# Kernel optimization log

Measured on AMD Instinct MI355X. Metric: run time of the kernel, lower is better.

Reference implementation:

```python
import jax, jax.numpy as jnp
import numpy as np
from jax import lax

B, T, IN, H = 16384, 10, 160, 256


def _lstm_layer(x, W_ih, W_hh, b_ih, b_hh):
    # x: [B, T, in]; PyTorch gate order: i, f, g, o. W_ih: [4H, in], W_hh: [4H, H]
    xg = jnp.einsum('bti,gi->btg', x, W_ih) + b_ih  # [B, T, 4H] precomputed input contributions
    h0 = jnp.zeros((x.shape[0], H), x.dtype)
    c0 = jnp.zeros((x.shape[0], H), x.dtype)

    def step(carry, xg_t):
        h, c = carry
        g = xg_t + h @ W_hh.T + b_hh  # [B, 4H]
        i, f, gg, o = jnp.split(g, 4, axis=-1)
        i = jax.nn.sigmoid(i)
        f = jax.nn.sigmoid(f)
        gg = jnp.tanh(gg)
        o = jax.nn.sigmoid(o)
        c = f * c + i * gg
        h = o * jnp.tanh(c)
        return (h, c), h

    _, hs = lax.scan(step, (h0, c0), xg.transpose(1, 0, 2))  # hs: [T, B, H]
    return hs.transpose(1, 0, 2)  # [B, T, H]


def setup_inputs() -> dict:
    key = jax.random.key(0)
    ks = jax.random.split(key, 11)
    s = 1.0 / np.sqrt(H)  # PyTorch default init scale
    inp = {
        'x': jax.random.normal(ks[0], (B, T, IN), jnp.float32),
        'W_ih0': jax.random.normal(ks[1], (4 * H, IN), jnp.float32) * s,
        'W_hh0': jax.random.normal(ks[2], (4 * H, H), jnp.float32) * s,
        'b_ih0': jax.random.normal(ks[3], (4 * H,), jnp.float32) * s,
        'b_hh0': jax.random.normal(ks[4], (4 * H,), jnp.float32) * s,
        'W_ih1': jax.random.normal(ks[5], (4 * H, H), jnp.float32) * s,
        'W_hh1': jax.random.normal(ks[6], (4 * H, H), jnp.float32) * s,
        'b_ih1': jax.random.normal(ks[7], (4 * H,), jnp.float32) * s,
        'b_hh1': jax.random.normal(ks[8], (4 * H,), jnp.float32) * s,
        'W_fc': jax.random.normal(ks[9], (1, T * H), jnp.float32) * 0.02,
        'b_fc': jax.random.normal(ks[10], (1,), jnp.float32) * 0.02,
    }
    return inp


def reference(x, W_ih0, W_hh0, b_ih0, b_hh0, W_ih1, W_hh1, b_ih1, b_hh1, W_fc, b_fc):
    x = x.reshape(-1, T, IN)
    h1 = _lstm_layer(x, W_ih0, W_hh0, b_ih0, b_hh0)   # [B, T, H]
    h2 = _lstm_layer(h1, W_ih1, W_hh1, b_ih1, b_hh1)  # [B, T, H]
    flat = h2.reshape(-1, T * H)                      # [B, 2560]
    logits = flat @ W_fc.T + b_fc                     # [B, 1]
    return jax.nn.sigmoid(logits)
```

## Files before the change

kernel.cpp:

```cpp
#include <hip/hip_runtime.h>

#define NTHREADS 512

typedef __attribute__((ext_vector_type(8))) short s16x8;
typedef __attribute__((ext_vector_type(4))) float f32x4;
typedef __attribute__((ext_vector_type(4))) unsigned int u32x4;

__device__ __forceinline__ unsigned short f2bf(float f) {
  unsigned u = __float_as_uint(f);
  u += 0x7fffu + ((u >> 16) & 1u);
  return (unsigned short)(u >> 16);
}
__device__ __forceinline__ float bf2f(unsigned short s) {
  return __uint_as_float(((unsigned)s) << 16);
}
__device__ __forceinline__ float sigm(float x) {
  return __builtin_amdgcn_rcpf(1.0f + __expf(-x));
}
__device__ __forceinline__ float tanh_fast(float x) {
  return 1.0f - 2.0f * __builtin_amdgcn_rcpf(1.0f + __expf(2.0f * x));
}
__device__ __forceinline__ f32x4 mfma_bf16(u32x4 a, u32x4 b, f32x4 c) {
  union { u32x4 u; s16x8 s; } ua, ub;
  ua.u = a; ub.u = b;
  return __builtin_amdgcn_mfma_f32_16x16x32_bf16(ua.s, ub.s, c, 0, 0, 0);
}

__global__ void pack_weights(const float* __restrict__ Wih0, const float* __restrict__ Whh0,
                             const float* __restrict__ bih0, const float* __restrict__ bhh0,
                             const float* __restrict__ Wih1, const float* __restrict__ Whh1,
                             const float* __restrict__ bih1, const float* __restrict__ bhh1,
                             unsigned short* __restrict__ W0p, unsigned short* __restrict__ W1p,
                             float* __restrict__ b0, float* __restrict__ b1) {
  int e = blockIdx.x * 256 + threadIdx.x;
  const int N0 = 16 * 52 * 4 * 128;
  const int N1 = 16 * 64 * 4 * 128;
  if (e < N0) {
    int kk = e & 7, t1 = e >> 3;
    int n = t1 & 15, t2 = t1 >> 4;
    int g = t2 & 3, t3 = t2 >> 2;
    int kb = t3 % 52, nb = t3 / 52;
    int gn = g * 256 + nb * 16 + n, k = kb * 8 + kk;
    float v = (k < 160) ? Wih0[gn * 160 + k] : Whh0[gn * 256 + (k - 160)];
    W0p[e] = f2bf(v);
  } else if (e < N0 + N1) {
    int e2 = e - N0;
    int kk = e2 & 7, t1 = e2 >> 3;
    int n = t1 & 15, t2 = t1 >> 4;
    int g = t2 & 3, t3 = t2 >> 2;
    int kb = t3 & 63, nb = t3 >> 6;
    int gn = g * 256 + nb * 16 + n, k = kb * 8 + kk;
    float v = (k < 256) ? Wih1[gn * 256 + k] : Whh1[gn * 256 + (k - 256)];
    W1p[e2] = f2bf(v);
  } else if (e < N0 + N1 + 1024) {
    int n = e - (N0 + N1);
    b0[n] = bih0[n] + bhh0[n];
  } else if (e < N0 + N1 + 2048) {
    int n = e - (N0 + N1 + 1024);
    b1[n] = bih1[n] + bhh1[n];
  }
}

__device__ __forceinline__ void ld4(u32x4 d[4], const u32x4* p) {
  d[0] = p[0]; d[1] = p[16]; d[2] = p[32]; d[3] = p[48];
}
__device__ __forceinline__ void mfma16(const u32x4 a[4], const u32x4 b[4],
                                       f32x4 acc[4][4]) {
#pragma unroll
  for (int g = 0; g < 4; g++)
#pragma unroll
    for (int rt = 0; rt < 4; rt++)
      acc[g][rt] = mfma_bf16(a[rt], b[g], acc[g][rt]);
}
template <int N>
__device__ __forceinline__ void kloop(const u32x4*& ap, const u32x4*& wp,
                                      f32x4 acc[4][4]) {
  u32x4 a0[4], b0[4], a1[4], b1[4];
  ld4(a0, ap); ld4(b0, wp); ap += 256; wp += 256;
#pragma unroll 1
  for (int i = 0; i < (N - 1) / 2; i++) {
    ld4(a1, ap); ld4(b1, wp); ap += 256; wp += 256;
    mfma16(a0, b0, acc);
    ld4(a0, ap); ld4(b0, wp); ap += 256; wp += 256;
    mfma16(a1, b1, acc);
  }
  if constexpr ((N & 1) == 0) {
    ld4(a1, ap); ld4(b1, wp); ap += 256; wp += 256;
    mfma16(a0, b0, acc);
    mfma16(a1, b1, acc);
  } else {
    mfma16(a0, b0, acc);
  }
}

__global__ __attribute__((amdgpu_flat_work_group_size(NTHREADS, NTHREADS),
                          amdgpu_waves_per_eu(2, 2)))
void lstm_fused(const float* __restrict__ x,
                const unsigned short* __restrict__ W0p,
                const unsigned short* __restrict__ W1p,
                const float* __restrict__ b0,
                const float* __restrict__ b1,
                const float* __restrict__ Wfc,
                const float* __restrict__ bfc,
                float* __restrict__ out) {
  __shared__ unsigned int lds_x[20 * 64 * 4];
  __shared__ unsigned int lds_h1[16384];
  __shared__ unsigned int lds_h2[16384];
  __shared__ float lds_red[512];
  __shared__ float lds_b0[1024];
  __shared__ float lds_b1[1024];

  const int tid = threadIdx.x;
  const int wave = tid >> 6;
  const int lane = tid & 63;
  const int l15 = lane & 15;
  const int quad = lane >> 4;
  const long rowg0 = (long)blockIdx.x * 64;

  for (int i = tid; i < 16384; i += NTHREADS) { lds_h1[i] = 0u; lds_h2[i] = 0u; }
  for (int i = tid; i < 1024; i += NTHREADS) { lds_b0[i] = b0[i]; lds_b1[i] = b1[i]; }

  float c0A[4][4], c0B[4][4], c2A[4][4], c2B[4][4];
#pragma unroll
  for (int rt = 0; rt < 4; rt++)
#pragma unroll
    for (int r = 0; r < 4; r++) {
      c0A[rt][r] = 0.f; c0B[rt][r] = 0.f;
      c2A[rt][r] = 0.f; c2B[rt][r] = 0.f;
    }
  float fc_acc = 0.0f;

  const u32x4* lxs = (const u32x4*)lds_x;
  const u32x4* lh1 = (const u32x4*)lds_h1;
  const u32x4* lh2 = (const u32x4*)lds_h2;
  unsigned short* lh1s = (unsigned short*)lds_h1;
  unsigned short* lh2s = (unsigned short*)lds_h2;
  const u32x4* w0q = (const u32x4*)W0p;
  const u32x4* w1q = (const u32x4*)W1p;

  for (int t = 0; t < 10; t++) {
    const int rd = t & 1;
    const int wr = rd ^ 1;

#pragma unroll
    for (int s = 0; s < 5; s++) {
      int p = tid + s * NTHREADS;
      int row = p / 40;
      int kq = p - row * 40;
      const f32x4 v = __builtin_nontemporal_load(
          (const f32x4*)(x + (rowg0 + row) * 1600 + t * 160 + kq * 4));
      unsigned lo = (unsigned)f2bf(v[0]) | ((unsigned)f2bf(v[1]) << 16);
      unsigned hi = (unsigned)f2bf(v[2]) | ((unsigned)f2bf(v[3]) << 16);
      int base = (kq >> 1) * 256 + row * 4 + (kq & 1) * 2;
      lds_x[base] = lo;
      lds_x[base + 1] = hi;
    }
    __syncthreads();

#pragma unroll 1
    for (int jt = 0; jt < 2; jt++) {
      const int nbb = wave * 2 + jt;
      f32x4 acc[4][4];
#pragma unroll
      for (int g = 0; g < 4; g++)
#pragma unroll
        for (int rt = 0; rt < 4; rt++) acc[g][rt] = (f32x4){0.f, 0.f, 0.f, 0.f};

      const u32x4* wp = w0q + (nbb * 52 + quad) * 64 + l15;
      const u32x4* ap = lxs + quad * 64 + l15;
      kloop<5>(ap, wp, acc);
      ap = lh1 + rd * 2048 + quad * 64 + l15;
      kloop<8>(ap, wp, acc);

      float b_i = lds_b0[0 * 256 + wave * 32 + jt * 16 + l15];
      float b_f = lds_b0[1 * 256 + wave * 32 + jt * 16 + l15];
      float b_g = lds_b0[2 * 256 + wave * 32 + jt * 16 + l15];
      float b_o = lds_b0[3 * 256 + wave * 32 + jt * 16 + l15];
#pragma unroll
      for (int rt = 0; rt < 4; rt++)
#pragma unroll
        for (int r = 0; r < 4; r++) {
          float iv = sigm(acc[0][rt][r] + b_i);
          float fv = sigm(acc[1][rt][r] + b_f);
          float gv = tanh_fast(acc[2][rt][r] + b_g);
          float ov = sigm(acc[3][rt][r] + b_o);
          float cn = fv * c0A[rt][r] + iv * gv;
          c0A[rt][r] = cn;
          int row = rt * 16 + quad * 4 + r;
          int col = wave * 32 + jt * 16 + l15;
          lh1s[wr * 16384 + ((col >> 3) * 64 + row) * 8 + (col & 7)] =
              f2bf(ov * tanh_fast(cn));
        }
#pragma unroll
      for (int rt = 0; rt < 4; rt++)
#pragma unroll
        for (int r = 0; r < 4; r++) {
          float tmp = c0A[rt][r]; c0A[rt][r] = c0B[rt][r]; c0B[rt][r] = tmp;
        }
    }
    __syncthreads();

#pragma unroll 1
    for (int jt = 0; jt < 2; jt++) {
      const int nbb = wave * 2 + jt;
      f32x4 acc[4][4];
#pragma unroll
      for (int g = 0; g < 4; g++)
#pragma unroll
        for (int rt = 0; rt < 4; rt++) acc[g][rt] = (f32x4){0.f, 0.f, 0.f, 0.f};

      const u32x4* wp = w1q + (nbb * 64 + quad) * 64 + l15;
      const u32x4* ap = lh1 + wr * 2048 + quad * 64 + l15;
      kloop<8>(ap, wp, acc);
      ap = lh2 + rd * 2048 + quad * 64 + l15;
      kloop<8>(ap, wp, acc);

      float b_i = lds_b1[0 * 256 + wave * 32 + jt * 16 + l15];
      float b_f = lds_b1[1 * 256 + wave * 32 + jt * 16 + l15];
      float b_g = lds_b1[2 * 256 + wave * 32 + jt * 16 + l15];
      float b_o = lds_b1[3 * 256 + wave * 32 + jt * 16 + l15];
#pragma unroll
      for (int rt = 0; rt < 4; rt++)
#pragma unroll
        for (int r = 0; r < 4; r++) {
          float iv = sigm(acc[0][rt][r] + b_i);
          float fv = sigm(acc[1][rt][r] + b_f);
          float gv = tanh_fast(acc[2][rt][r] + b_g);
          float ov = sigm(acc[3][rt][r] + b_o);
          float cn = fv * c2A[rt][r] + iv * gv;
          c2A[rt][r] = cn;
          int row = rt * 16 + quad * 4 + r;
          int col = wave * 32 + jt * 16 + l15;
          lh2s[wr * 16384 + ((col >> 3) * 64 + row) * 8 + (col & 7)] =
              f2bf(ov * tanh_fast(cn));
        }
#pragma unroll
      for (int rt = 0; rt < 4; rt++)
#pragma unroll
        for (int r = 0; r < 4; r++) {
          float tmp = c2A[rt][r]; c2A[rt][r] = c2B[rt][r]; c2B[rt][r] = tmp;
        }
    }
    __syncthreads();

    {
      int row = tid >> 3;
      int jq = (tid & 7) * 32;
      float s = 0.f;
#pragma unroll
      for (int kb = 0; kb < 4; kb++) {
        u32x4 hv = lh2[wr * 2048 + ((jq >> 3) + kb) * 64 + row];
        const f32x4 wA = *(const f32x4*)(Wfc + t * 256 + jq + kb * 8);
        const f32x4 wB = *(const f32x4*)(Wfc + t * 256 + jq + kb * 8 + 4);
#pragma unroll
        for (int e = 0; e < 2; e++) {
          unsigned u = hv[e];
          s += bf2f((unsigned short)(u & 0xffffu)) * wA[2 * e];
          s += bf2f((unsigned short)(u >> 16)) * wA[2 * e + 1];
        }
#pragma unroll
        for (int e = 0; e < 2; e++) {
          unsigned u = hv[2 + e];
          s += bf2f((unsigned short)(u & 0xffffu)) * wB[2 * e];
          s += bf2f((unsigned short)(u >> 16)) * wB[2 * e + 1];
        }
      }
      fc_acc += s;
    }
  }

  lds_red[tid] = fc_acc;
  __syncthreads();
  if (tid < 64) {
    float s = 0.f;
#pragma unroll
    for (int e = 0; e < 8; e++) s += lds_red[tid * 8 + e];
    out[rowg0 + tid] = sigm(s + bfc[0]);
  }
}

extern "C" void kernel_launch(void* const* d_in, const int* in_sizes, int n_in,
                              void* d_out, int out_size, void* d_ws, size_t ws_size,
                              hipStream_t stream) {
  const float* x    = (const float*)d_in[0];
  const float* Wih0 = (const float*)d_in[1];
  const float* Whh0 = (const float*)d_in[2];
  const float* bih0 = (const float*)d_in[3];
  const float* bhh0 = (const float*)d_in[4];
  const float* Wih1 = (const float*)d_in[5];
  const float* Whh1 = (const float*)d_in[6];
  const float* bih1 = (const float*)d_in[7];
  const float* bhh1 = (const float*)d_in[8];
  const float* Wfc  = (const float*)d_in[9];
  const float* bfc  = (const float*)d_in[10];
  float* out = (float*)d_out;

  unsigned short* W0p = (unsigned short*)d_ws;
  unsigned short* W1p = W0p + 16 * 52 * 4 * 128;
  float* b0 = (float*)(W1p + 16 * 64 * 4 * 128);
  float* b1 = b0 + 1024;

  const int total = 16 * 52 * 4 * 128 + 16 * 64 * 4 * 128 + 2048;
  pack_weights<<<(total + 255) / 256, 256, 0, stream>>>(
      Wih0, Whh0, bih0, bhh0, Wih1, Whh1, bih1, bhh1, W0p, W1p, b0, b1);
  lstm_fused<<<256, NTHREADS, 0, stream>>>(x, W0p, W1p, b0, b1, Wfc, bfc, out);
}
```

Measured before the change: 494.6 us.

## Halve rows per block to 32 and launch 512 blocks with higher occupancy

Each workgroup now processes 32 batch rows instead of 64, so the grid doubles to 512 blocks and LDS use is roughly halved. Biases are stored in LDS as packed bf16, and the reduction buffer reuses the x staging area, so two blocks fit per CU (waves_per_eu raised to 4). The aim is to fill all CUs and overlap latency across blocks. In exchange, each block streams the full packed weights from L2 for only half the rows, which doubles weight traffic per useful MFMA. Rounding the biases to bf16 also slightly changes numerics.

Result: slower. 569.7 us (+15.2%).

```diff
diff --git a/kernel.cpp b/kernel.cpp
--- a/kernel.cpp
+++ b/kernel.cpp
@@ -24,6 +24,10 @@
   union { u32x4 u; s16x8 s; } ua, ub;
   ua.u = a; ub.u = b;
   return __builtin_amdgcn_mfma_f32_16x16x32_bf16(ua.s, ub.s, c, 0, 0, 0);
+}
+__device__ __forceinline__ float ldsb(const unsigned* p, int idx) {
+  unsigned u = p[idx >> 1];
+  return bf2f((unsigned short)((idx & 1) ? (u >> 16) : (u & 0xffffu)));
 }
 
 __global__ void pack_weights(const float* __restrict__ Wih0, const float* __restrict__ Whh0,
@@ -64,37 +68,37 @@
 __device__ __forceinline__ void ld4(u32x4 d[4], const u32x4* p) {
   d[0] = p[0]; d[1] = p[16]; d[2] = p[32]; d[3] = p[48];
 }
-__device__ __forceinline__ void mfma16(const u32x4 a[4], const u32x4 b[4],
-                                       f32x4 acc[4][4]) {
-#pragma unroll
-  for (int g = 0; g < 4; g++)
-#pragma unroll
-    for (int rt = 0; rt < 4; rt++)
-      acc[g][rt] = mfma_bf16(a[rt], b[g], acc[g][rt]);
+__device__ __forceinline__ void mfma8(u32x4 a0, u32x4 a1, const u32x4 b[4],
+                                      f32x4 acc[4][2]) {
+#pragma unroll
+  for (int g = 0; g < 4; g++) {
+    acc[g][0] = mfma_bf16(a0, b[g], acc[g][0]);
+    acc[g][1] = mfma_bf16(a1, b[g], acc[g][1]);
+  }
 }
 template <int N>
-__device__ __forceinline__ void kloop(const u32x4*& ap, const u32x4*& wp,
-                                      f32x4 acc[4][4]) {
-  u32x4 a0[4], b0[4], a1[4], b1[4];
-  ld4(a0, ap); ld4(b0, wp); ap += 256; wp += 256;
+__device__ __forceinline__ void kloop32(const u32x4*& ap, const u32x4*& wp,
+                                        f32x4 acc[4][2]) {
+  u32x4 b0[4], b1[4];
+  ld4(b0, wp); wp += 256;
 #pragma unroll 1
   for (int i = 0; i < (N - 1) / 2; i++) {
-    ld4(a1, ap); ld4(b1, wp); ap += 256; wp += 256;
-    mfma16(a0, b0, acc);
-    ld4(a0, ap); ld4(b0, wp); ap += 256; wp += 256;
-    mfma16(a1, b1, acc);
+    ld4(b1, wp); wp += 256;
+    { u32x4 a0 = ap[0], a1 = ap[16]; ap += 128; mfma8(a0, a1, b0, acc); }
+    ld4(b0, wp); wp += 256;
+    { u32x4 a0 = ap[0], a1 = ap[16]; ap += 128; mfma8(a0, a1, b1, acc); }
   }
   if constexpr ((N & 1) == 0) {
-    ld4(a1, ap); ld4(b1, wp); ap += 256; wp += 256;
-    mfma16(a0, b0, acc);
-    mfma16(a1, b1, acc);
+    ld4(b1, wp); wp += 256;
+    { u32x4 a0 = ap[0], a1 = ap[16]; ap += 128; mfma8(a0, a1, b0, acc); }
+    { u32x4 a0 = ap[0], a1 = ap[16]; ap += 128; mfma8(a0, a1, b1, acc); }
   } else {
-    mfma16(a0, b0, acc);
+    { u32x4 a0 = ap[0], a1 = ap[16]; ap += 128; mfma8(a0, a1, b0, acc); }
   }
 }
 
 __global__ __attribute__((amdgpu_flat_work_group_size(NTHREADS, NTHREADS),
-                          amdgpu_waves_per_eu(2, 2)))
+                          amdgpu_waves_per_eu(4, 4)))
 void lstm_fused(const float* __restrict__ x,
                 const unsigned short* __restrict__ W0p,
                 const unsigned short* __restrict__ W1p,
@@ -103,26 +107,28 @@
                 const float* __restrict__ Wfc,
                 const float* __restrict__ bfc,
                 float* __restrict__ out) {
-  __shared__ unsigned int lds_x[20 * 64 * 4];
-  __shared__ unsigned int lds_h1[16384];
-  __shared__ unsigned int lds_h2[16384];
-  __shared__ float lds_red[512];
-  __shared__ float lds_b0[1024];
-  __shared__ float lds_b1[1024];
+  __shared__ unsigned int lds_x[2560];
+  __shared__ unsigned int lds_h1[8192];
+  __shared__ unsigned int lds_h2[8192];
+  __shared__ unsigned int lds_b0u[512];
+  __shared__ unsigned int lds_b1u[512];
 
   const int tid = threadIdx.x;
   const int wave = tid >> 6;
   const int lane = tid & 63;
   const int l15 = lane & 15;
   const int quad = lane >> 4;
-  const long rowg0 = (long)blockIdx.x * 64;
-
-  for (int i = tid; i < 16384; i += NTHREADS) { lds_h1[i] = 0u; lds_h2[i] = 0u; }
-  for (int i = tid; i < 1024; i += NTHREADS) { lds_b0[i] = b0[i]; lds_b1[i] = b1[i]; }
-
-  float c0A[4][4], c0B[4][4], c2A[4][4], c2B[4][4];
-#pragma unroll
-  for (int rt = 0; rt < 4; rt++)
+  const long rowg0 = (long)blockIdx.x * 32;
+
+  for (int i = tid; i < 8192; i += NTHREADS) { lds_h1[i] = 0u; lds_h2[i] = 0u; }
+  {
+    lds_b0u[tid] = (unsigned)f2bf(b0[2 * tid]) | ((unsigned)f2bf(b0[2 * tid + 1]) << 16);
+    lds_b1u[tid] = (unsigned)f2bf(b1[2 * tid]) | ((unsigned)f2bf(b1[2 * tid + 1]) << 16);
+  }
+
+  float c0A[2][4], c0B[2][4], c2A[2][4], c2B[2][4];
+#pragma unroll
+  for (int rt = 0; rt < 2; rt++)
 #pragma unroll
     for (int r = 0; r < 4; r++) {
       c0A[rt][r] = 0.f; c0B[rt][r] = 0.f;
@@ -143,41 +149,44 @@
     const int wr = rd ^ 1;
 
 #pragma unroll
-    for (int s = 0; s < 5; s++) {
+    for (int s = 0; s < 3; s++) {
       int p = tid + s * NTHREADS;
-      int row = p / 40;
-      int kq = p - row * 40;
-      const f32x4 v = __builtin_nontemporal_load(
-          (const f32x4*)(x + (rowg0 + row) * 1600 + t * 160 + kq * 4));
-      unsigned lo = (unsigned)f2bf(v[0]) | ((unsigned)f2bf(v[1]) << 16);
-      unsigned hi = (unsigned)f2bf(v[2]) | ((unsigned)f2bf(v[3]) << 16);
-      int base = (kq >> 1) * 256 + row * 4 + (kq & 1) * 2;
-      lds_x[base] = lo;
-      lds_x[base + 1] = hi;
+      if (p < 1280) {
+        int row = p / 40;
+        int kq = p - row * 40;
+        const f32x4 v = __builtin_nontemporal_load(
+            (const f32x4*)(x + (rowg0 + row) * 1600 + t * 160 + kq * 4));
+        unsigned lo = (unsigned)f2bf(v[0]) | ((unsigned)f2bf(v[1]) << 16);
+        unsigned hi = (unsigned)f2bf(v[2]) | ((unsigned)f2bf(v[3]) << 16);
+        int base = (kq >> 1) * 128 + row * 4 + (kq & 1) * 2;
+        lds_x[base] = lo;
+        lds_x[base + 1] = hi;
+      }
     }
     __syncthreads();
 
 #pragma unroll 1
     for (int jt = 0; jt < 2; jt++) {
       const int nbb = wave * 2 + jt;
-      f32x4 acc[4][4];
+      f32x4 acc[4][2];
 #pragma unroll
       for (int g = 0; g < 4; g++)
 #pragma unroll
-        for (int rt = 0; rt < 4; rt++) acc[g][rt] = (f32x4){0.f, 0.f, 0.f, 0.f};
+        for (int rt = 0; rt < 2; rt++) acc[g][rt] = (f32x4){0.f, 0.f, 0.f, 0.f};
 
       const u32x4* wp = w0q + (nbb * 52 + quad) * 64 + l15;
-      const u32x4* ap = lxs + quad * 64 + l15;
-      kloop<5>(ap, wp, acc);
-      ap = lh1 + rd * 2048 + quad * 64 + l15;
-      kloop<8>(ap, wp, acc);
-
-      float b_i = lds_b0[0 * 256 + wave * 32 + jt * 16 + l15];
-      float b_f = lds_b0[1 * 256 + wave * 32 + jt * 16 + l15];
-      float b_g = lds_b0[2 * 256 + wave * 32 + jt * 16 + l15];
-      float b_o = lds_b0[3 * 256 + wave * 32 + jt * 16 + l15];
-#pragma unroll
-      for (int rt = 0; rt < 4; rt++)
+      const u32x4* ap = lxs + quad * 32 + l15;
+      kloop32<5>(ap, wp, acc);
+      ap = lh1 + rd * 1024 + quad * 32 + l15;
+      kloop32<8>(ap, wp, acc);
+
+      const int col = wave * 32 + jt * 16 + l15;
+      float b_i = ldsb(lds_b0u, 0 * 256 + col);
+      float b_f = ldsb(lds_b0u, 1 * 256 + col);
+      float b_g = ldsb(lds_b0u, 2 * 256 + col);
+      float b_o = ldsb(lds_b0u, 3 * 256 + col);
+#pragma unroll
+      for (int rt = 0; rt < 2; rt++)
 #pragma unroll
         for (int r = 0; r < 4; r++) {
           float iv = sigm(acc[0][rt][r] + b_i);
@@ -187,12 +196,11 @@
           float cn = fv * c0A[rt][r] + iv * gv;
           c0A[rt][r] = cn;
           int row = rt * 16 + quad * 4 + r;
-          int col = wave * 32 + jt * 16 + l15;
-          lh1s[wr * 16384 + ((col >> 3) * 64 + row) * 8 + (col & 7)] =
+          lh1s[wr * 8192 + ((col >> 3) * 32 + row) * 8 + (col & 7)] =
               f2bf(ov * tanh_fast(cn));
         }
 #pragma unroll
-      for (int rt = 0; rt < 4; rt++)
+      for (int rt = 0; rt < 2; rt++)
 #pragma unroll
         for (int r = 0; r < 4; r++) {
           float tmp = c0A[rt][r]; c0A[rt][r] = c0B[rt][r]; c0B[rt][r] = tmp;
@@ -203,24 +211,25 @@
 #pragma unroll 1
     for (int jt = 0; jt < 2; jt++) {
       const int nbb = wave * 2 + jt;
-      f32x4 acc[4][4];
+      f32x4 acc[4][2];
 #pragma unroll
       for (int g = 0; g < 4; g++)
 #pragma unroll
-        for (int rt = 0; rt < 4; rt++) acc[g][rt] = (f32x4){0.f, 0.f, 0.f, 0.f};
+        for (int rt = 0; rt < 2; rt++) acc[g][rt] = (f32x4){0.f, 0.f, 0.f, 0.f};
 
       const u32x4* wp = w1q + (nbb * 64 + quad) * 64 + l15;
-      const u32x4* ap = lh1 + wr * 2048 + quad * 64 + l15;
-      kloop<8>(ap, wp, acc);
-      ap = lh2 + rd * 2048 + quad * 64 + l15;
-      kloop<8>(ap, wp, acc);
-
-      float b_i = lds_b1[0 * 256 + wave * 32 + jt * 16 + l15];
-      float b_f = lds_b1[1 * 256 + wave * 32 + jt * 16 + l15];
-      float b_g = lds_b1[2 * 256 + wave * 32 + jt * 16 + l15];
-      float b_o = lds_b1[3 * 256 + wave * 32 + jt * 16 + l15];
-#pragma unroll
-      for (int rt = 0; rt < 4; rt++)
+      const u32x4* ap = lh1 + wr * 1024 + quad * 32 + l15;
+      kloop32<8>(ap, wp, acc);
+      ap = lh2 + rd * 1024 + quad * 32 + l15;
+      kloop32<8>(ap, wp, acc);
+
+      const int col = wave * 32 + jt * 16 + l15;
+      float b_i = ldsb(lds_b1u, 0 * 256 + col);
+      float b_f = ldsb(lds_b1u, 1 * 256 + col);
+      float b_g = ldsb(lds_b1u, 2 * 256 + col);
+      float b_o = ldsb(lds_b1u, 3 * 256 + col);
+#pragma unroll
+      for (int rt = 0; rt < 2; rt++)
 #pragma unroll
         for (int r = 0; r < 4; r++) {
           float iv = sigm(acc[0][rt][r] + b_i);
@@ -230,12 +239,11 @@
           float cn = fv * c2A[rt][r] + iv * gv;
           c2A[rt][r] = cn;
           int row = rt * 16 + quad * 4 + r;
-          int col = wave * 32 + jt * 16 + l15;
-          lh2s[wr * 16384 + ((col >> 3) * 64 + row) * 8 + (col & 7)] =
+          lh2s[wr * 8192 + ((col >> 3) * 32 + row) * 8 + (col & 7)] =
               f2bf(ov * tanh_fast(cn));
         }
 #pragma unroll
-      for (int rt = 0; rt < 4; rt++)
+      for (int rt = 0; rt < 2; rt++)
 #pragma unroll
         for (int r = 0; r < 4; r++) {
           float tmp = c2A[rt][r]; c2A[rt][r] = c2B[rt][r]; c2B[rt][r] = tmp;
@@ -244,14 +252,14 @@
     __syncthreads();
 
     {
-      int row = tid >> 3;
-      int jq = (tid & 7) * 32;
+      int row = tid >> 4;
+      int slot = tid & 15;
       float s = 0.f;
 #pragma unroll
-      for (int kb = 0; kb < 4; kb++) {
-        u32x4 hv = lh2[wr * 2048 + ((jq >> 3) + kb) * 64 + row];
-        const f32x4 wA = *(const f32x4*)(Wfc + t * 256 + jq + kb * 8);
-        const f32x4 wB = *(const f32x4*)(Wfc + t * 256 + jq + kb * 8 + 4);
+      for (int kb = 0; kb < 2; kb++) {
+        u32x4 hv = lh2[wr * 1024 + (slot * 2 + kb) * 32 + row];
+        const f32x4 wA = *(const f32x4*)(Wfc + t * 256 + slot * 16 + kb * 8);
+        const f32x4 wB = *(const f32x4*)(Wfc + t * 256 + slot * 16 + kb * 8 + 4);
 #pragma unroll
         for (int e = 0; e < 2; e++) {
           unsigned u = hv[e];
@@ -269,12 +277,13 @@
     }
   }
 
-  lds_red[tid] = fc_acc;
+  float* lds_redp = (float*)lds_x;
+  lds_redp[tid] = fc_acc;
   __syncthreads();
-  if (tid < 64) {
+  if (tid < 32) {
     float s = 0.f;
 #pragma unroll
-    for (int e = 0; e < 8; e++) s += lds_red[tid * 8 + e];
+    for (int e = 0; e < 16; e++) s += lds_redp[tid * 16 + e];
     out[rowg0 + tid] = sigm(s + bfc[0]);
   }
 }
@@ -303,5 +312,5 @@
   const int total = 16 * 52 * 4 * 128 + 16 * 64 * 4 * 128 + 2048;
   pack_weights<<<(total + 255) / 256, 256, 0, stream>>>(
       Wih0, Whh0, bih0, bhh0, Wih1, Whh1, bih1, bhh1, W0p, W1p, b0, b1);
-  lstm_fused<<<256, NTHREADS, 0, stream>>>(x, W0p, W1p, b0, b1, Wfc, bfc, out);
-}
+  lstm_fused<<<512, NTHREADS, 0, stream>>>(x, W0p, W1p, b0, b1, Wfc, bfc, out);
+}
```
